# Kernel tuning notes

Measured on AMD Instinct MI355X. Metric: run time of the kernel, lower is better.

The kernel has to match this reference:

```python
import jax, jax.numpy as jnp
import numpy as np

N_NODES = 100000
N_EDGES = 1600000
IN_CH = 64
OUT_CH = 32
HEADS = 4
NEG_SLOPE = 0.2


def setup_inputs() -> dict:
    key = jax.random.key(0)
    k = jax.random.split(key, 6)
    x = jax.random.normal(k[0], (N_NODES, IN_CH), dtype=jnp.float32)
    edge_index = jax.random.randint(k[1], (2, N_EDGES), 0, N_NODES, dtype=jnp.int32)
    W = jax.random.normal(k[2], (IN_CH, HEADS * OUT_CH), dtype=jnp.float32) * 0.1
    att_src = jax.random.normal(k[3], (1, HEADS, OUT_CH), dtype=jnp.float32) * 0.1
    att_dst = jax.random.normal(k[4], (1, HEADS, OUT_CH), dtype=jnp.float32) * 0.1
    bias = jnp.zeros((HEADS * OUT_CH,), dtype=jnp.float32)
    return {"x": x, "edge_index": edge_index, "W": W,
            "att_src": att_src, "att_dst": att_dst, "bias": bias}


def reference(x, edge_index, W, att_src, att_dst, bias):
    N = x.shape[0]
    H, C = att_src.shape[1], att_src.shape[2]
    # GATConv defaults: add self loops
    loop = jnp.arange(N, dtype=edge_index.dtype)
    src = jnp.concatenate([edge_index[0], loop])  # [E+N]
    dst = jnp.concatenate([edge_index[1], loop])  # [E+N]
    # linear transform -> [N, H, C]
    h = (x @ W).reshape(N, H, C)
    # per-node attention halves: [N, H]
    a_src = jnp.sum(h * att_src, axis=-1)
    a_dst = jnp.sum(h * att_dst, axis=-1)
    # edge scores with LeakyReLU: [E+N, H]
    e = jax.nn.leaky_relu(a_src[src] + a_dst[dst], negative_slope=NEG_SLOPE)
    # segment softmax over destination nodes (numerically stable)
    m = jax.ops.segment_max(e, dst, num_segments=N)           # [N, H]
    m = jnp.where(jnp.isfinite(m), m, 0.0)
    ex = jnp.exp(e - m[dst])                                   # [E+N, H]
    denom = jax.ops.segment_sum(ex, dst, num_segments=N)      # [N, H]
    alpha = ex / (denom[dst] + 1e-16)                          # [E+N, H]
    # scatter-aggregate weighted source features -> [N, H, C]
    out = jax.ops.segment_sum(h[src] * alpha[:, :, None], dst, num_segments=N)
    out = out.reshape(N, H * C) + bias
    return jax.nn.log_softmax(out, axis=1)
```

## Files before the change

### kernel.cpp

```cpp
#include <hip/hip_runtime.h>
#include <hip/hip_bf16.h>

#define IN_CH 64
#define HC 128
#define NHEAD 4
#define NEG 0.2f
#define CAPB 64
#define NB 250
#define BWID 400
#define CAP2 8192
#define CH1 4096
#define VPT 8

typedef short s16x8 __attribute__((ext_vector_type(8)));
typedef float f32x4 __attribute__((ext_vector_type(4)));

__device__ __forceinline__ float leaky(float v) { return v >= 0.f ? v : NEG * v; }
__device__ __forceinline__ float bf2f(unsigned short u) {
    return __uint_as_float(((unsigned int)u) << 16);
}
__device__ __forceinline__ unsigned short f2bf(float f) {
    unsigned int u = __float_as_uint(f);
    u += 0x7fff + ((u >> 16) & 1);
    return (unsigned short)(u >> 16);
}

__global__ void __launch_bounds__(256) k_prep(
        const float* __restrict__ W, const float* __restrict__ att_src,
        const float* __restrict__ att_dst, float* __restrict__ usd) {
    const int t = threadIdx.x;
    for (int idx = t; idx < 16 * 64; idx += 256) {
        const int j = idx >> 6, k = idx & 63;
        float v = 0.f;
        if (j < 8) {
            const int h = j & 3;
            const float* att = (j < 4) ? att_src : att_dst;
#pragma unroll
            for (int c = 0; c < 32; ++c)
                v += W[k * HC + h * 32 + c] * att[h * 32 + c];
        }
        usd[idx] = v;
    }
}

__global__ void __launch_bounds__(256) k_xform(
        const float* __restrict__ x, const float* __restrict__ W,
        const float* __restrict__ usd,
        unsigned short* __restrict__ h_bf, float* __restrict__ a_src,
        float* __restrict__ a_dst, int N) {
    __shared__ unsigned short xs[128][72];
    __shared__ unsigned short wt[144][72];
    const int t = threadIdx.x;
    const int rowbase_blk = blockIdx.x * 128;

    for (int idx = t; idx < (IN_CH * HC) / 4; idx += 256) {
        const float4 v = ((const float4*)W)[idx];
        const int k = idx >> 5;
        const int c0 = (idx & 31) * 4;
        wt[c0 + 0][k] = f2bf(v.x);
        wt[c0 + 1][k] = f2bf(v.y);
        wt[c0 + 2][k] = f2bf(v.z);
        wt[c0 + 3][k] = f2bf(v.w);
    }
    for (int idx = t; idx < 16 * 64; idx += 256) {
        wt[128 + (idx >> 6)][idx & 63] = f2bf(usd[idx]);
    }
    for (int idx = t; idx < (128 * IN_CH) / 4; idx += 256) {
        const int row = idx >> 4;
        const int c0 = (idx & 15) * 4;
        const int grow = min(rowbase_blk + row, N - 1);
        const float4 v = ((const float4*)(x + (size_t)grow * IN_CH))[idx & 15];
        const unsigned int p0 = (unsigned int)f2bf(v.x) | ((unsigned int)f2bf(v.y) << 16);
        const unsigned int p1 = (unsigned int)f2bf(v.z) | ((unsigned int)f2bf(v.w) << 16);
        *(uint2*)&xs[row][c0] = make_uint2(p0, p1);
    }
    __syncthreads();

    const int lane = t & 63;
    const int w = t >> 6;
    const int rbase = w * 32;
    const int lr = lane & 15, lq = lane >> 4;

    f32x4 acc[2][9];
#pragma unroll
    for (int m = 0; m < 2; ++m)
#pragma unroll
        for (int n = 0; n < 9; ++n) acc[m][n] = (f32x4){0.f, 0.f, 0.f, 0.f};

#pragma unroll
    for (int ks = 0; ks < 2; ++ks) {
        const s16x8 a0 = *(const s16x8*)&xs[rbase + lr][ks * 32 + lq * 8];
        const s16x8 a1 = *(const s16x8*)&xs[rbase + 16 + lr][ks * 32 + lq * 8];
#pragma unroll
        for (int n = 0; n < 9; ++n) {
            const s16x8 b = *(const s16x8*)&wt[n * 16 + lr][ks * 32 + lq * 8];
            acc[0][n] = __builtin_amdgcn_mfma_f32_16x16x32_bf16(a0, b, acc[0][n], 0, 0, 0);
            acc[1][n] = __builtin_amdgcn_mfma_f32_16x16x32_bf16(a1, b, acc[1][n], 0, 0, 0);
        }
    }

#pragma unroll
    for (int m = 0; m < 2; ++m) {
#pragma unroll
        for (int j = 0; j < 4; ++j) {
            const int grow = rowbase_blk + rbase + m * 16 + lq * 4 + j;
            if (grow >= N) continue;
#pragma unroll
            for (int n = 0; n < 8; ++n)
                h_bf[(size_t)grow * HC + n * 16 + lr] = f2bf(acc[m][n][j]);
            const float av = acc[m][8][j];
            if (lr < 4) a_src[grow * NHEAD + lr] = av;
            else if (lr < 8) a_dst[grow * NHEAD + (lr - 4)] = av;
        }
    }
}

__global__ void __launch_bounds__(512) k_bin(
        const int* __restrict__ src, const int* __restrict__ dst,
        int* __restrict__ bcnt, int* __restrict__ pairs, int E) {
    __shared__ int hist[NB];
    __shared__ int scanbuf[256];
    __shared__ int startb[NB];
    __shared__ int gbase[NB];
    __shared__ int lbuf[CH1];
    __shared__ int gposb[CH1];

    const int t = threadIdx.x;
    const int base = blockIdx.x * CH1;
    const int cnt = min(CH1, E - base);

    for (int i = t; i < NB; i += 512) hist[i] = 0;
    __syncthreads();

    int pk[VPT]; int rb[VPT];
#pragma unroll
    for (int k = 0; k < VPT; ++k) {
        const int idx = base + k * 512 + t;
        if (idx < E) {
            const int s = src[idx], d = dst[idx];
            const int b = d / BWID;
            const int dl = d - b * BWID;
            pk[k] = (dl << 17) | s;
            const int rank = atomicAdd(&hist[b], 1);
            rb[k] = (b << 16) | rank;
        } else {
            pk[k] = 0; rb[k] = -1;
        }
    }
    __syncthreads();

    if (t < 256) scanbuf[t] = (t < NB) ? hist[t] : 0;
    __syncthreads();
    for (int off = 1; off < 256; off <<= 1) {
        int add = 0;
        if (t < 256 && t >= off) add = scanbuf[t - off];
        __syncthreads();
        if (t < 256) scanbuf[t] += add;
        __syncthreads();
    }
    if (t < NB) {
        const int h = hist[t];
        startb[t] = scanbuf[t] - h;
        gbase[t] = (h > 0) ? atomicAdd(&bcnt[t * 16], h) : 0;
    }
    __syncthreads();

#pragma unroll
    for (int k = 0; k < VPT; ++k) {
        if (rb[k] >= 0) {
            const int b = rb[k] >> 16;
            const int rank = rb[k] & 0xffff;
            const int lpos = startb[b] + rank;
            const int gp = gbase[b] + rank;
            lbuf[lpos] = pk[k];
            gposb[lpos] = (gp < CAP2) ? (b * CAP2 + gp) : -1;
        }
    }
    __syncthreads();

    for (int i = t; i < cnt; i += 512) {
        const int g = gposb[i];
        if (g >= 0) pairs[g] = lbuf[i];
    }
}

__global__ void __launch_bounds__(512) k_fill(
        const int* __restrict__ bcnt, const int* __restrict__ pairs,
        int* __restrict__ srcbuf, int* __restrict__ rowstart,
        int* __restrict__ deg) {
    const int b = blockIdx.x;
    const int t = threadIdx.x;
    __shared__ int scnt[BWID];
    __shared__ int sstart[BWID];
    __shared__ int cur[BWID];
    __shared__ int scan2[512];
    __shared__ int slist[CAP2];
    __shared__ int sbase;

    int part = 0;
    for (int i = t; i < b; i += 512) part += min(bcnt[i * 16], CAP2);
    scan2[t] = part; __syncthreads();
    for (int off = 256; off > 0; off >>= 1) {
        if (t < off) scan2[t] += scan2[t + off];
        __syncthreads();
    }
    if (t == 0) sbase = scan2[0];

    for (int i = t; i < BWID; i += 512) scnt[i] = 0;
    __syncthreads();

    const int mc = min(bcnt[b * 16], CAP2);
    const int pb = b * CAP2;

    for (int i = t; i < mc; i += 512)
        atomicAdd(&scnt[pairs[pb + i] >> 17], 1);
    __syncthreads();

    scan2[t] = (t < BWID) ? scnt[t] : 0;
    __syncthreads();
    for (int off = 1; off < 512; off <<= 1) {
        const int add = (t >= off) ? scan2[t - off] : 0;
        __syncthreads();
        scan2[t] += add;
        __syncthreads();
    }
    if (t < BWID) {
        const int ex = scan2[t] - scnt[t];
        sstart[t] = ex; cur[t] = ex;
        rowstart[b * BWID + t] = sbase + ex;
        deg[b * BWID + t] = scnt[t];
    }
    __syncthreads();

    for (int i = t; i < mc; i += 512) {
        const int e = pairs[pb + i];
        const int p = atomicAdd(&cur[e >> 17], 1);
        slist[p] = e & 0x1ffff;
    }
    __syncthreads();

    for (int i = t; i < mc; i += 512) srcbuf[sbase + i] = slist[i];
}

__global__ void __launch_bounds__(256) k_node(
        const int* __restrict__ deg_, const int* __restrict__ rowstart,
        const int* __restrict__ srcbuf,
        const float* __restrict__ a_src, const float* __restrict__ a_dst,
        const unsigned short* __restrict__ h_bf, const float* __restrict__ bias,
        float* __restrict__ out, int N) {
    const int lane = threadIdx.x & 63;
    const int w = threadIdx.x >> 6;
    int n = blockIdx.x * 4 + w;
    n = min(n, N - 1);
    const int deg = deg_[n];
    const int start = rowstart[n];
    const int myh = lane & 3;

    __shared__ float s_ex[4][CAPB * NHEAD];
    __shared__ int   s_src[4][CAPB];

    const float ad  = a_dst[n * NHEAD + myh];
    const float asf = a_src[n * NHEAD + myh];

    float mxas = asf;
    for (int j = lane >> 2; j < deg; j += 16) {
        const int s = srcbuf[start + j];
        const float as = a_src[s * NHEAD + myh];
        if (j < CAPB) {
            s_ex[w][j * NHEAD + myh] = as;
            if (myh == 0) s_src[w][j] = s;
        }
        mxas = fmaxf(mxas, as);
    }
#pragma unroll
    for (int off = 4; off < 64; off <<= 1) mxas = fmaxf(mxas, __shfl_xor(mxas, off, 64));
    const float m = leaky(mxas + ad);
    __syncthreads();

    float sm = (lane < 4) ? __expf(leaky(asf + ad) - m) : 0.f;
    for (int j = lane >> 2; j < deg; j += 16) {
        const float as = (j < CAPB) ? s_ex[w][j * NHEAD + myh]
                                    : a_src[srcbuf[start + j] * NHEAD + myh];
        const float ex = __expf(leaky(as + ad) - m);
        if (j < CAPB) s_ex[w][j * NHEAD + myh] = ex;
        sm += ex;
    }
#pragma unroll
    for (int off = 4; off < 64; off <<= 1) sm += __shfl_xor(sm, off, 64);
    const float r = 1.f / (sm + 1e-16f);
    __syncthreads();

    const int hh = lane >> 4;
    const float rh  = __shfl(r, hh, 64);
    const float mh  = __shfl(m, hh, 64);
    const float adh = __shfl(ad, hh, 64);

    const int dcap = min(deg, CAPB);
    float acc0 = 0.f, acc1 = 0.f;
    for (int j = 0; j < dcap; ++j) {
        const int s = s_src[w][j];
        const float al = s_ex[w][j * NHEAD + hh] * rh;
        const ushort2 hv = *((const ushort2*)(h_bf + (size_t)s * HC) + lane);
        acc0 = fmaf(al, bf2f(hv.x), acc0);
        acc1 = fmaf(al, bf2f(hv.y), acc1);
    }
    for (int j = CAPB; j < deg; ++j) {
        const int s = srcbuf[start + j];
        const float al = __expf(leaky(a_src[s * NHEAD + hh] + adh) - mh) * rh;
        const ushort2 hv = *((const ushort2*)(h_bf + (size_t)s * HC) + lane);
        acc0 = fmaf(al, bf2f(hv.x), acc0);
        acc1 = fmaf(al, bf2f(hv.y), acc1);
    }
    {
        const float als = __expf(leaky(asf + ad) - m) * r;
        const float alh = __shfl(als, hh, 64);
        const ushort2 hv = *((const ushort2*)(h_bf + (size_t)n * HC) + lane);
        acc0 = fmaf(alh, bf2f(hv.x), acc0);
        acc1 = fmaf(alh, bf2f(hv.y), acc1);
    }

    float v0 = acc0 + bias[2 * lane];
    float v1 = acc1 + bias[2 * lane + 1];
    float mxv = fmaxf(v0, v1);
#pragma unroll
    for (int off = 1; off < 64; off <<= 1) mxv = fmaxf(mxv, __shfl_xor(mxv, off, 64));
    float se = __expf(v0 - mxv) + __expf(v1 - mxv);
#pragma unroll
    for (int off = 1; off < 64; off <<= 1) se += __shfl_xor(se, off, 64);
    const float lse = mxv + __logf(se);
    float2* op = (float2*)(out + (size_t)n * HC) + lane;
    *op = make_float2(v0 - lse, v1 - lse);
}

extern "C" void kernel_launch(void* const* d_in, const int* in_sizes, int n_in,
                              void* d_out, int out_size, void* d_ws, size_t ws_size,
                              hipStream_t stream) {
    const float* x       = (const float*)d_in[0];
    const int*   ei      = (const int*)d_in[1];
    const float* W       = (const float*)d_in[2];
    const float* att_src = (const float*)d_in[3];
    const float* att_dst = (const float*)d_in[4];
    const float* bias    = (const float*)d_in[5];
    float* out = (float*)d_out;

    const int N = in_sizes[0] / IN_CH;
    const int E = in_sizes[1] / 2;
    const int* src = ei;
    const int* dst = ei + E;

    char* wsb = (char*)d_ws;
    unsigned short* h_bf = (unsigned short*)wsb;    wsb += (size_t)N * HC * 2;
    float* a_src  = (float*)wsb;                    wsb += (size_t)N * NHEAD * 4;
    float* a_dst  = (float*)wsb;                    wsb += (size_t)N * NHEAD * 4;
    int*   bcnt   = (int*)wsb;                      wsb += (size_t)NB * 16 * 4;
    int*   pairs  = (int*)wsb;                      wsb += (size_t)NB * CAP2 * 4;
    int*   srcbuf = (int*)wsb;                      wsb += (size_t)E * 4;
    int*   rowstart = (int*)wsb;                    wsb += (size_t)N * 4;
    int*   deg    = (int*)wsb;                      wsb += (size_t)N * 4;
    float* usd    = (float*)wsb;                    wsb += 16 * 64 * 4;

    hipMemsetAsync(bcnt, 0, (size_t)NB * 16 * 4, stream);

    k_prep<<<1, 256, 0, stream>>>(W, att_src, att_dst, usd);
    k_xform<<<(N + 127) / 128, 256, 0, stream>>>(x, W, usd, h_bf, a_src, a_dst, N);
    k_bin<<<(E + CH1 - 1) / CH1, 512, 0, stream>>>(src, dst, bcnt, pairs, E);
    k_fill<<<NB, 512, 0, stream>>>(bcnt, pairs, srcbuf, rowstart, deg);
    k_node<<<(N + 3) / 4, 256, 0, stream>>>(deg, rowstart, srcbuf,
                                            a_src, a_dst,
                                            (const unsigned short*)h_bf, bias, out, N);
}
```

Before: 227.3 us.

## Restructure node aggregation to process four edges per wave with vectorized loads

The per-node aggregation kernel now gives each lane one edge and loads all four head scores as a float4. It replaces the per-head shuffled reductions with full-wave float4 reductions. The gather loop handles four edges at once per wave, with 16-lane groups each loading 8 bf16 channels via uint4, then reduces across the groups and defers the softmax normalization to the end. The tiny k_prep kernel is folded into k_xform, which removes one launch, but every xform block now recomputes the attention-projection weights.

```diff
diff --git a/kernel.cpp b/kernel.cpp
--- a/kernel.cpp
+++ b/kernel.cpp
@@ -15,37 +15,36 @@
 typedef short s16x8 __attribute__((ext_vector_type(8)));
 typedef float f32x4 __attribute__((ext_vector_type(4)));
 
-__device__ __forceinline__ float leaky(float v) { return v >= 0.f ? v : NEG * v; }
-__device__ __forceinline__ float bf2f(unsigned short u) {
-    return __uint_as_float(((unsigned int)u) << 16);
-}
+__device__ __forceinline__ float leaky(float v) { return fmaxf(v, NEG * v); }
 __device__ __forceinline__ unsigned short f2bf(float f) {
     unsigned int u = __float_as_uint(f);
     u += 0x7fff + ((u >> 16) & 1);
     return (unsigned short)(u >> 16);
 }
-
-__global__ void __launch_bounds__(256) k_prep(
-        const float* __restrict__ W, const float* __restrict__ att_src,
-        const float* __restrict__ att_dst, float* __restrict__ usd) {
-    const int t = threadIdx.x;
-    for (int idx = t; idx < 16 * 64; idx += 256) {
-        const int j = idx >> 6, k = idx & 63;
-        float v = 0.f;
-        if (j < 8) {
-            const int h = j & 3;
-            const float* att = (j < 4) ? att_src : att_dst;
-#pragma unroll
-            for (int c = 0; c < 32; ++c)
-                v += W[k * HC + h * 32 + c] * att[h * 32 + c];
-        }
-        usd[idx] = v;
-    }
+__device__ __forceinline__ float4 fmax4(float4 a, float4 b) {
+    return make_float4(fmaxf(a.x, b.x), fmaxf(a.y, b.y), fmaxf(a.z, b.z), fmaxf(a.w, b.w));
+}
+__device__ __forceinline__ float4 add4(float4 a, float4 b) {
+    return make_float4(a.x + b.x, a.y + b.y, a.z + b.z, a.w + b.w);
+}
+__device__ __forceinline__ float4 leaky4(float4 v) {
+    return make_float4(leaky(v.x), leaky(v.y), leaky(v.z), leaky(v.w));
+}
+__device__ __forceinline__ float4 expm4(float4 v, float4 m) {
+    return make_float4(__expf(v.x - m.x), __expf(v.y - m.y),
+                       __expf(v.z - m.z), __expf(v.w - m.w));
+}
+__device__ __forceinline__ float comp4(float4 v, int i) {
+    float r = v.x;
+    r = (i == 1) ? v.y : r;
+    r = (i == 2) ? v.z : r;
+    r = (i == 3) ? v.w : r;
+    return r;
 }
 
 __global__ void __launch_bounds__(256) k_xform(
         const float* __restrict__ x, const float* __restrict__ W,
-        const float* __restrict__ usd,
+        const float* __restrict__ att_src, const float* __restrict__ att_dst,
         unsigned short* __restrict__ h_bf, float* __restrict__ a_src,
         float* __restrict__ a_dst, int N) {
     __shared__ unsigned short xs[128][72];
@@ -63,7 +62,16 @@
         wt[c0 + 3][k] = f2bf(v.w);
     }
     for (int idx = t; idx < 16 * 64; idx += 256) {
-        wt[128 + (idx >> 6)][idx & 63] = f2bf(usd[idx]);
+        const int j = idx >> 6, k = idx & 63;
+        float v = 0.f;
+        if (j < 8) {
+            const int h = j & 3;
+            const float* att = (j < 4) ? att_src : att_dst;
+#pragma unroll
+            for (int c = 0; c < 32; ++c)
+                v += W[k * HC + h * 32 + c] * att[h * 32 + c];
+        }
+        wt[128 + j][k] = f2bf(v);
     }
     for (int idx = t; idx < (128 * IN_CH) / 4; idx += 256) {
         const int row = idx >> 4;
@@ -254,82 +262,144 @@
     n = min(n, N - 1);
     const int deg = deg_[n];
     const int start = rowstart[n];
-    const int myh = lane & 3;
-
-    __shared__ float s_ex[4][CAPB * NHEAD];
+    const int dcap = min(deg, CAPB);
+
+    __shared__ float s_ex[4][CAPB][NHEAD];
     __shared__ int   s_src[4][CAPB];
 
-    const float ad  = a_dst[n * NHEAD + myh];
-    const float asf = a_src[n * NHEAD + myh];
-
-    float mxas = asf;
-    for (int j = lane >> 2; j < deg; j += 16) {
+    const float4 ad4  = *(const float4*)(a_dst + n * NHEAD);
+    const float4 asn4 = *(const float4*)(a_src + n * NHEAD);
+
+    float4 mx4 = asn4;
+    int myS = -1;
+    float4 as4 = asn4;
+    if (lane < dcap) {
+        myS = srcbuf[start + lane];
+        as4 = *(const float4*)(a_src + myS * NHEAD);
+        s_src[w][lane] = myS;
+        mx4 = fmax4(mx4, as4);
+    }
+    for (int j = CAPB + lane; j < deg; j += 64) {
         const int s = srcbuf[start + j];
-        const float as = a_src[s * NHEAD + myh];
-        if (j < CAPB) {
-            s_ex[w][j * NHEAD + myh] = as;
-            if (myh == 0) s_src[w][j] = s;
-        }
-        mxas = fmaxf(mxas, as);
-    }
-#pragma unroll
-    for (int off = 4; off < 64; off <<= 1) mxas = fmaxf(mxas, __shfl_xor(mxas, off, 64));
-    const float m = leaky(mxas + ad);
-    __syncthreads();
-
-    float sm = (lane < 4) ? __expf(leaky(asf + ad) - m) : 0.f;
-    for (int j = lane >> 2; j < deg; j += 16) {
-        const float as = (j < CAPB) ? s_ex[w][j * NHEAD + myh]
-                                    : a_src[srcbuf[start + j] * NHEAD + myh];
-        const float ex = __expf(leaky(as + ad) - m);
-        if (j < CAPB) s_ex[w][j * NHEAD + myh] = ex;
-        sm += ex;
-    }
-#pragma unroll
-    for (int off = 4; off < 64; off <<= 1) sm += __shfl_xor(sm, off, 64);
-    const float r = 1.f / (sm + 1e-16f);
-    __syncthreads();
-
-    const int hh = lane >> 4;
-    const float rh  = __shfl(r, hh, 64);
-    const float mh  = __shfl(m, hh, 64);
-    const float adh = __shfl(ad, hh, 64);
-
-    const int dcap = min(deg, CAPB);
-    float acc0 = 0.f, acc1 = 0.f;
-    for (int j = 0; j < dcap; ++j) {
-        const int s = s_src[w][j];
-        const float al = s_ex[w][j * NHEAD + hh] * rh;
-        const ushort2 hv = *((const ushort2*)(h_bf + (size_t)s * HC) + lane);
-        acc0 = fmaf(al, bf2f(hv.x), acc0);
-        acc1 = fmaf(al, bf2f(hv.y), acc1);
-    }
-    for (int j = CAPB; j < deg; ++j) {
+        mx4 = fmax4(mx4, *(const float4*)(a_src + s * NHEAD));
+    }
+#pragma unroll
+    for (int off = 1; off < 64; off <<= 1) {
+        mx4.x = fmaxf(mx4.x, __shfl_xor(mx4.x, off, 64));
+        mx4.y = fmaxf(mx4.y, __shfl_xor(mx4.y, off, 64));
+        mx4.z = fmaxf(mx4.z, __shfl_xor(mx4.z, off, 64));
+        mx4.w = fmaxf(mx4.w, __shfl_xor(mx4.w, off, 64));
+    }
+    const float4 m4 = leaky4(add4(mx4, ad4));
+
+    float4 sum4 = make_float4(0.f, 0.f, 0.f, 0.f);
+    if (myS >= 0) {
+        const float4 e4 = expm4(leaky4(add4(as4, ad4)), m4);
+        *(float4*)&s_ex[w][lane][0] = e4;
+        sum4 = e4;
+    }
+    for (int j = CAPB + lane; j < deg; j += 64) {
         const int s = srcbuf[start + j];
-        const float al = __expf(leaky(a_src[s * NHEAD + hh] + adh) - mh) * rh;
-        const ushort2 hv = *((const ushort2*)(h_bf + (size_t)s * HC) + lane);
-        acc0 = fmaf(al, bf2f(hv.x), acc0);
-        acc1 = fmaf(al, bf2f(hv.y), acc1);
-    }
+        const float4 a = *(const float4*)(a_src + s * NHEAD);
+        sum4 = add4(sum4, expm4(leaky4(add4(a, ad4)), m4));
+    }
+#pragma unroll
+    for (int off = 1; off < 64; off <<= 1) {
+        sum4.x += __shfl_xor(sum4.x, off, 64);
+        sum4.y += __shfl_xor(sum4.y, off, 64);
+        sum4.z += __shfl_xor(sum4.z, off, 64);
+        sum4.w += __shfl_xor(sum4.w, off, 64);
+    }
+    const float4 self4 = expm4(leaky4(add4(asn4, ad4)), m4);
+    sum4 = add4(sum4, self4);
+    const float4 r4 = make_float4(1.f / (sum4.x + 1e-16f), 1.f / (sum4.y + 1e-16f),
+                                  1.f / (sum4.z + 1e-16f), 1.f / (sum4.w + 1e-16f));
+
+    const int cg = lane >> 4;
+    const int cl = lane & 15;
+    const int hd = cl >> 2;
+    float acc[8];
+#pragma unroll
+    for (int k = 0; k < 8; ++k) acc[k] = 0.f;
+
+    for (int j0 = 0; j0 < dcap; j0 += 4) {
+        const int j = j0 + cg;
+        float al = 0.f; int s = 0;
+        if (j < dcap) { s = s_src[w][j]; al = s_ex[w][j][hd]; }
+        const uint4 hv = *(const uint4*)(h_bf + (size_t)s * HC + cl * 8);
+        acc[0] = fmaf(al, __uint_as_float(hv.x << 16), acc[0]);
+        acc[1] = fmaf(al, __uint_as_float(hv.x & 0xffff0000u), acc[1]);
+        acc[2] = fmaf(al, __uint_as_float(hv.y << 16), acc[2]);
+        acc[3] = fmaf(al, __uint_as_float(hv.y & 0xffff0000u), acc[3]);
+        acc[4] = fmaf(al, __uint_as_float(hv.z << 16), acc[4]);
+        acc[5] = fmaf(al, __uint_as_float(hv.z & 0xffff0000u), acc[5]);
+        acc[6] = fmaf(al, __uint_as_float(hv.w << 16), acc[6]);
+        acc[7] = fmaf(al, __uint_as_float(hv.w & 0xffff0000u), acc[7]);
+    }
+    for (int j0 = CAPB; j0 < deg; j0 += 4) {
+        const int j = j0 + cg;
+        float al = 0.f; int s = 0;
+        if (j < deg) {
+            s = srcbuf[start + j];
+            const float4 a = *(const float4*)(a_src + s * NHEAD);
+            al = comp4(expm4(leaky4(add4(a, ad4)), m4), hd);
+        }
+        const uint4 hv = *(const uint4*)(h_bf + (size_t)s * HC + cl * 8);
+        acc[0] = fmaf(al, __uint_as_float(hv.x << 16), acc[0]);
+        acc[1] = fmaf(al, __uint_as_float(hv.x & 0xffff0000u), acc[1]);
+        acc[2] = fmaf(al, __uint_as_float(hv.y << 16), acc[2]);
+        acc[3] = fmaf(al, __uint_as_float(hv.y & 0xffff0000u), acc[3]);
+        acc[4] = fmaf(al, __uint_as_float(hv.z << 16), acc[4]);
+        acc[5] = fmaf(al, __uint_as_float(hv.z & 0xffff0000u), acc[5]);
+        acc[6] = fmaf(al, __uint_as_float(hv.w << 16), acc[6]);
+        acc[7] = fmaf(al, __uint_as_float(hv.w & 0xffff0000u), acc[7]);
+    }
+
+#pragma unroll
+    for (int k = 0; k < 8; ++k) {
+        acc[k] += __shfl_xor(acc[k], 16, 64);
+        acc[k] += __shfl_xor(acc[k], 32, 64);
+    }
+
     {
-        const float als = __expf(leaky(asf + ad) - m) * r;
-        const float alh = __shfl(als, hh, 64);
-        const ushort2 hv = *((const ushort2*)(h_bf + (size_t)n * HC) + lane);
-        acc0 = fmaf(alh, bf2f(hv.x), acc0);
-        acc1 = fmaf(alh, bf2f(hv.y), acc1);
-    }
-
-    float v0 = acc0 + bias[2 * lane];
-    float v1 = acc1 + bias[2 * lane + 1];
-    float mxv = fmaxf(v0, v1);
-#pragma unroll
-    for (int off = 1; off < 64; off <<= 1) mxv = fmaxf(mxv, __shfl_xor(mxv, off, 64));
-    float se = __expf(v0 - mxv) + __expf(v1 - mxv);
-#pragma unroll
-    for (int off = 1; off < 64; off <<= 1) se += __shfl_xor(se, off, 64);
+        const float als = comp4(self4, hd);
+        const uint4 hv = *(const uint4*)(h_bf + (size_t)n * HC + cl * 8);
+        acc[0] = fmaf(als, __uint_as_float(hv.x << 16), acc[0]);
+        acc[1] = fmaf(als, __uint_as_float(hv.x & 0xffff0000u), acc[1]);
+        acc[2] = fmaf(als, __uint_as_float(hv.y << 16), acc[2]);
+        acc[3] = fmaf(als, __uint_as_float(hv.y & 0xffff0000u), acc[3]);
+        acc[4] = fmaf(als, __uint_as_float(hv.z << 16), acc[4]);
+        acc[5] = fmaf(als, __uint_as_float(hv.z & 0xffff0000u), acc[5]);
+        acc[6] = fmaf(als, __uint_as_float(hv.w << 16), acc[6]);
+        acc[7] = fmaf(als, __uint_as_float(hv.w & 0xffff0000u), acc[7]);
+    }
+
+    const float rsel = comp4(r4, hd);
+    const float4 b0 = *(const float4*)(bias + cl * 8);
+    const float4 b1 = *(const float4*)(bias + cl * 8 + 4);
+    acc[0] = acc[0] * rsel + b0.x; acc[1] = acc[1] * rsel + b0.y;
+    acc[2] = acc[2] * rsel + b0.z; acc[3] = acc[3] * rsel + b0.w;
+    acc[4] = acc[4] * rsel + b1.x; acc[5] = acc[5] * rsel + b1.y;
+    acc[6] = acc[6] * rsel + b1.z; acc[7] = acc[7] * rsel + b1.w;
+
+    float mxv = acc[0];
+#pragma unroll
+    for (int k = 1; k < 8; ++k) mxv = fmaxf(mxv, acc[k]);
+#pragma unroll
+    for (int off = 1; off < 16; off <<= 1) mxv = fmaxf(mxv, __shfl_xor(mxv, off, 64));
+    float se = 0.f;
+#pragma unroll
+    for (int k = 0; k < 8; ++k) se += __expf(acc[k] - mxv);
+#pragma unroll
+    for (int off = 1; off < 16; off <<= 1) se += __shfl_xor(se, off, 64);
     const float lse = mxv + __logf(se);
-    float2* op = (float2*)(out + (size_t)n * HC) + lane;
-    *op = make_float2(v0 - lse, v1 - lse);
+
+    if (lane < 32) {
+        const int hi = lane >> 4;
+        float4 o = make_float4(acc[hi * 4 + 0] - lse, acc[hi * 4 + 1] - lse,
+                               acc[hi * 4 + 2] - lse, acc[hi * 4 + 3] - lse);
+        *(float4*)(out + (size_t)n * HC + cl * 8 + hi * 4) = o;
+    }
 }
 
 extern "C" void kernel_launch(void* const* d_in, const int* in_sizes, int n_in,
@@ -357,12 +427,11 @@
     int*   srcbuf = (int*)wsb;                      wsb += (size_t)E * 4;
     int*   rowstart = (int*)wsb;                    wsb += (size_t)N * 4;
     int*   deg    = (int*)wsb;                      wsb += (size_t)N * 4;
-    float* usd    = (float*)wsb;                    wsb += 16 * 64 * 4;
 
     hipMemsetAsync(bcnt, 0, (size_t)NB * 16 * 4, stream);
 
-    k_prep<<<1, 256, 0, stream>>>(W, att_src, att_dst, usd);
-    k_xform<<<(N + 127) / 128, 256, 0, stream>>>(x, W, usd, h_bf, a_src, a_dst, N);
+    k_xform<<<(N + 127) / 128, 256, 0, stream>>>(x, W, att_src, att_dst,
+                                                 h_bf, a_src, a_dst, N);
     k_bin<<<(E + CH1 - 1) / CH1, 512, 0, stream>>>(src, dst, bcnt, pairs, E);
     k_fill<<<NB, 512, 0, stream>>>(bcnt, pairs, srcbuf, rowstart, deg);
     k_node<<<(N + 3) / 4, 256, 0, stream>>>(deg, rowstart, srcbuf,
```

After: 234.1 us. 1.03x slower.
